# Kernel tuning notes

Hardware: AMD Instinct MI355X
Metric: run time of the kernel (lower is better)

Reference implementation:

```python
import jax, jax.numpy as jnp
import numpy as np

H = 64        # index_n_heads
D = 128       # index_head_dim
R = 64        # rope_head_dim
TOPK = 512    # index_topk
FP8_MAX = 448.0
EPS = 1e-6
THETA = 10000.0


def setup_inputs() -> dict:
    key = jax.random.key(0)
    ks = jax.random.split(key, 6)
    T, DM, QL = 1536, 7168, 1536
    return {
        "hidden_states": jax.random.normal(ks[0], (T, DM), jnp.float32),
        "q_lora": jax.random.normal(ks[1], (T, QL), jnp.float32),
        "wq_b": jax.random.normal(ks[2], (QL, H * D), jnp.float32) / np.sqrt(QL),
        "wk": jax.random.normal(ks[3], (DM, D), jnp.float32) / np.sqrt(DM),
        "k_norm_w": jnp.ones((D,), jnp.float32),
        "k_norm_b": jnp.zeros((D,), jnp.float32),
        "weights_proj_w": jax.random.normal(ks[4], (DM, H), jnp.float32) / np.sqrt(DM),
        "positions": jnp.arange(T, dtype=jnp.int32),
    }


def _rope_neox(x, pos):
    # x: [T, ..., R]; pos: [T]. NEOX-style (half-split) rotary on the rope slice.
    half = R // 2
    inv = 1.0 / (THETA ** (jnp.arange(half, dtype=jnp.float32) / half))
    ang = pos.astype(jnp.float32)[:, None] * inv  # [T, half]
    cos, sin = jnp.cos(ang), jnp.sin(ang)
    while cos.ndim < x.ndim:
        cos, sin = cos[:, None, :], sin[:, None, :]
    x1, x2 = x[..., :half], x[..., half:]
    return jnp.concatenate([x1 * cos - x2 * sin, x2 * cos + x1 * sin], axis=-1)


def _fp8_quant(x):
    # per-row (last-dim) e4m3 quantization: value -> fp8 payload + fp32 scale
    scale = jnp.maximum(jnp.max(jnp.abs(x), axis=-1, keepdims=True) / FP8_MAX, 1e-12)
    xq = (x / scale).astype(jnp.float8_e4m3fn).astype(jnp.float32)
    return xq, scale


def reference(hidden_states, q_lora, wq_b, wk, k_norm_w, k_norm_b, weights_proj_w, positions):
    T = hidden_states.shape[0]
    softmax_scale = D ** (-0.5)
    weights_scale = H ** (-0.5)

    # projections
    q = (q_lora @ wq_b).reshape(T, H, D)          # wq_b
    k = hidden_states @ wk                        # wk

    # k_norm (LayerNorm)
    mu = jnp.mean(k, axis=-1, keepdims=True)
    var = jnp.mean((k - mu) ** 2, axis=-1, keepdims=True)
    k = (k - mu) * jax.lax.rsqrt(var + EPS) * k_norm_w + k_norm_b

    # RoPE on the first rope_head_dim dims of q and k
    q = jnp.concatenate([_rope_neox(q[..., :R], positions), q[..., R:]], axis=-1)
    k = jnp.concatenate([_rope_neox(k[..., :R], positions), k[..., R:]], axis=-1)

    # fp8 quantization (per token-head for q, per token for k)
    q_fp8, q_scale = _fp8_quant(q)   # [T,H,D], [T,H,1]
    k_fp8, k_scale = _fp8_quant(k)   # [T,D],   [T,1]

    # head-gate weights: weights_proj(x) * q_scale * softmax_scale * weights_scale
    gate = hidden_states @ weights_proj_w                      # [T,H]
    w = gate[..., None] * q_scale * (softmax_scale * weights_scale)  # [T,H,1]

    # index score: I[t,s] = sum_h w[t,h] * relu(q[t,h] . k[s]) * k_scale[s]
    qk = jnp.einsum('thd,sd->ths', q_fp8, k_fp8)               # [T,H,S]
    score = jnp.einsum('th,ths->ts', w[..., 0], jax.nn.relu(qk))
    score = score * k_scale[:, 0][None, :]

    # causal (ragged prefill) mask + topk block selection
    causal = positions[:, None] >= positions[None, :]
    score = jnp.where(causal, score, -jnp.inf)
    vals, idx = jax.lax.top_k(score, TOPK)
    idx = jnp.where(jnp.isfinite(vals), idx, -1)
    return idx, vals
```

## Files before the change

### kernel.cpp

```cpp
#include <hip/hip_runtime.h>
#include <hip/hip_bf16.h>
#include <math.h>

#define T_SZ 1536
#define DM_SZ 7168
#define QL_SZ 1536
#define H_SZ 64
#define D_SZ 128
#define ND 8192
#define TOPK_SZ 512
#define N2 192
#define SPLITK2 16

typedef float f32x4 __attribute__((ext_vector_type(4)));
typedef short s16x8 __attribute__((ext_vector_type(8)));
typedef unsigned long long u64;

static __device__ __forceinline__ unsigned char f32_to_e4m3(float x){
  unsigned int b = __float_as_uint(x);
  unsigned int s = (b >> 24) & 0x80u;
  float a = fabsf(x);
  if (a < 0.015625f){
    int m = (int)rintf(a * 512.0f);
    if (m == 8) return (unsigned char)(s | 0x08u);
    return (unsigned char)(s | (unsigned)m);
  }
  int e;
  float mant = frexpf(a, &e);
  int E = e - 1;
  int m = (int)rintf(mant * 16.0f) - 8;
  if (m == 8){ E += 1; m = 0; }
  if (E > 8 || (E == 8 && m > 6)) return (unsigned char)(s | 0x7Eu);
  return (unsigned char)(s | ((unsigned)(E + 7) << 3) | (unsigned)m);
}

static __device__ __forceinline__ unsigned short bf16_rne(float x){
  unsigned int u = __float_as_uint(x);
  return (unsigned short)((u + 0x7FFFu + ((u >> 16) & 1u)) >> 16);
}

typedef __attribute__((address_space(1))) const void gas_void;
typedef __attribute__((address_space(3))) void las_void;
static __device__ __forceinline__ void stage16(const void* g, void* l){
  __builtin_amdgcn_global_load_lds((gas_void*)g, (las_void*)l, 16, 0, 0);
}

__global__ __launch_bounds__(256) void prep_all_k(const float* __restrict__ ql,
                                                  const float* __restrict__ wqb,
                                                  const float* __restrict__ wk,
                                                  const float* __restrict__ wp,
                                                  const int* __restrict__ pos,
                                                  unsigned short* __restrict__ Ahi,
                                                  unsigned short* __restrict__ Alo,
                                                  unsigned short* __restrict__ Bth,
                                                  unsigned short* __restrict__ Btl,
                                                  unsigned short* __restrict__ w2hi,
                                                  unsigned short* __restrict__ w2lo,
                                                  float* __restrict__ cs){
  __shared__ float ld[32][33];
  const int blk = blockIdx.x, tid = threadIdx.x;
  if (blk < 2304){
    int i = blk * 256 + tid;
    float4 v = *(const float4*)&ql[(size_t)i * 4];
    float f[4] = {v.x, v.y, v.z, v.w};
    unsigned short hb[4], lb[4];
#pragma unroll
    for (int j = 0; j < 4; ++j){
      hb[j] = bf16_rne(f[j]);
      float hf = __uint_as_float((unsigned int)hb[j] << 16);
      lb[j] = bf16_rne(f[j] - hf);
    }
    ushort4 h, l;
    h.x = hb[0]; h.y = hb[1]; h.z = hb[2]; h.w = hb[3];
    l.x = lb[0]; l.y = lb[1]; l.z = lb[2]; l.w = lb[3];
    *(ushort4*)&Ahi[(size_t)i * 4] = h;
    *(ushort4*)&Alo[(size_t)i * 4] = l;
  } else if (blk < 14592){
    int f2 = blk - 2304;
    const int n0 = (f2 & 255) * 32, k0 = (f2 >> 8) * 32;
    const int r = tid >> 3, c4 = (tid & 7) * 4;
    float4 v = *(const float4*)&wqb[(size_t)(k0 + r) * ND + n0 + c4];
    ld[r][c4 + 0] = v.x; ld[r][c4 + 1] = v.y; ld[r][c4 + 2] = v.z; ld[r][c4 + 3] = v.w;
    __syncthreads();
    unsigned short hb[4], lb[4];
#pragma unroll
    for (int j = 0; j < 4; ++j){
      float x = ld[c4 + j][r];
      hb[j] = bf16_rne(x);
      float hf = __uint_as_float((unsigned int)hb[j] << 16);
      lb[j] = bf16_rne(x - hf);
    }
    ushort4 h, l;
    h.x = hb[0]; h.y = hb[1]; h.z = hb[2]; h.w = hb[3];
    l.x = lb[0]; l.y = lb[1]; l.z = lb[2]; l.w = lb[3];
    *(ushort4*)&Bth[(size_t)(n0 + r) * QL_SZ + k0 + c4] = h;
    *(ushort4*)&Btl[(size_t)(n0 + r) * QL_SZ + k0 + c4] = l;
  } else if (blk < 15936){
    int g = blk - 14592;
    const int n0 = (g % 6) * 32, k0 = (g / 6) * 32;
    const int r = tid >> 3, c4 = (tid & 7) * 4;
    float4 v;
    if (n0 < 128) v = *(const float4*)&wk[(size_t)(k0 + r) * 128 + n0 + c4];
    else          v = *(const float4*)&wp[(size_t)(k0 + r) * 64 + (n0 - 128) + c4];
    ld[r][c4 + 0] = v.x; ld[r][c4 + 1] = v.y; ld[r][c4 + 2] = v.z; ld[r][c4 + 3] = v.w;
    __syncthreads();
    unsigned short hb[4], lb[4];
#pragma unroll
    for (int j = 0; j < 4; ++j){
      float x = ld[c4 + j][r];
      hb[j] = bf16_rne(x);
      float hf = __uint_as_float((unsigned int)hb[j] << 16);
      lb[j] = bf16_rne(x - hf);
    }
    ushort4 h, l;
    h.x = hb[0]; h.y = hb[1]; h.z = hb[2]; h.w = hb[3];
    l.x = lb[0]; l.y = lb[1]; l.z = lb[2]; l.w = lb[3];
    *(ushort4*)&w2hi[(size_t)(n0 + r) * DM_SZ + k0 + c4] = h;
    *(ushort4*)&w2lo[(size_t)(n0 + r) * DM_SZ + k0 + c4] = l;
  } else {
    int i = (blk - 15936) * 256 + tid;
    int t = i >> 5, j = i & 31;
    float inv = 1.0f / powf(10000.0f, (float)j * (1.0f / 32.0f));
    float ang = (float)pos[t] * inv;
    cs[t * 64 + j]      = cosf(ang);
    cs[t * 64 + 32 + j] = sinf(ang);
  }
}

__global__ void rope_table_k(const int* __restrict__ pos, float* __restrict__ cs){
  int i = blockIdx.x * blockDim.x + threadIdx.x;
  if (i >= T_SZ * 32) return;
  int t = i >> 5, j = i & 31;
  float inv = 1.0f / powf(10000.0f, (float)j * (1.0f / 32.0f));
  float ang = (float)pos[t] * inv;
  cs[t * 64 + j]      = cosf(ang);
  cs[t * 64 + 32 + j] = sinf(ang);
}

__global__ __launch_bounds__(256) void gemm1_mfma_k(const unsigned short* __restrict__ Ahi,
                                                    const unsigned short* __restrict__ Alo,
                                                    const unsigned short* __restrict__ Bhi,
                                                    const unsigned short* __restrict__ Blo,
                                                    float* __restrict__ C){
  __shared__ unsigned short As [128 * 64];
  __shared__ unsigned short Bs0[128 * 64];
  __shared__ unsigned short Bs1[128 * 64];
  const int bid = blockIdx.x;
  const int lid = (bid & 7) * 96 + (bid >> 3);
  const int mt = lid % 12, nt = lid / 12;
  const int m0 = mt * 128, n0 = nt * 128;
  const int tid = threadIdx.x;
  const int w = tid >> 6, l = tid & 63;
  const int wr = w >> 1, wc = w & 1;
  const int lr = l & 15, lg = l >> 4;

  const int srow = w * 32 + (l >> 3);
  const int ssl  = (l & 7) ^ ((l >> 3) & 7);
  const size_t gA = (size_t)(m0 + srow) * QL_SZ + ssl * 8;
  const size_t gB = (size_t)(n0 + srow) * QL_SZ + ssl * 8;
  const int lbase = w * 2048;

  f32x4 acc[4][4];
#pragma unroll
  for (int i = 0; i < 4; ++i)
#pragma unroll
    for (int j = 0; j < 4; ++j) acc[i][j] = (f32x4){0.f, 0.f, 0.f, 0.f};

  const int amrow = wr * 64 + lr;
  const int bnrow = wc * 64 + lr;

  for (int k0 = 0; k0 < QL_SZ; k0 += 64){
#pragma unroll
    for (int i = 0; i < 4; ++i){
      size_t go = (size_t)i * 8 * QL_SZ + k0;
      stage16(Ahi + gA + go, As  + lbase + i * 512);
      stage16(Bhi + gB + go, Bs0 + lbase + i * 512);
      stage16(Blo + gB + go, Bs1 + lbase + i * 512);
    }
    __syncthreads();
#pragma unroll
    for (int kk = 0; kk < 2; ++kk){
      s16x8 af[4], b0[4], b1[4];
#pragma unroll
      for (int f = 0; f < 4; ++f){
        int ma = amrow + f * 16;
        int nb = bnrow + f * 16;
        int sa = ((kk * 4 + lg) ^ (ma & 7)) * 16;
        int sb = ((kk * 4 + lg) ^ (nb & 7)) * 16;
        af[f] = *(const s16x8*)((const char*)As  + ma * 128 + sa);
        b0[f] = *(const s16x8*)((const char*)Bs0 + nb * 128 + sb);
        b1[f] = *(const s16x8*)((const char*)Bs1 + nb * 128 + sb);
      }
#pragma unroll
      for (int fi = 0; fi < 4; ++fi)
#pragma unroll
        for (int fj = 0; fj < 4; ++fj)
          acc[fi][fj] = __builtin_amdgcn_mfma_f32_16x16x32_bf16(af[fi], b0[fj], acc[fi][fj], 0, 0, 0);
#pragma unroll
      for (int fi = 0; fi < 4; ++fi)
#pragma unroll
        for (int fj = 0; fj < 4; ++fj)
          acc[fi][fj] = __builtin_amdgcn_mfma_f32_16x16x32_bf16(af[fi], b1[fj], acc[fi][fj], 0, 0, 0);
    }
    __syncthreads();
#pragma unroll
    for (int i = 0; i < 4; ++i)
      stage16(Alo + gA + (size_t)i * 8 * QL_SZ + k0, As + lbase + i * 512);
    __syncthreads();
#pragma unroll
    for (int kk = 0; kk < 2; ++kk){
      s16x8 af[4], b0[4];
#pragma unroll
      for (int f = 0; f < 4; ++f){
        int ma = amrow + f * 16;
        int nb = bnrow + f * 16;
        af[f] = *(const s16x8*)((const char*)As  + ma * 128 + (((kk * 4 + lg) ^ (ma & 7)) * 16));
        b0[f] = *(const s16x8*)((const char*)Bs0 + nb * 128 + (((kk * 4 + lg) ^ (nb & 7)) * 16));
      }
#pragma unroll
      for (int fi = 0; fi < 4; ++fi)
#pragma unroll
        for (int fj = 0; fj < 4; ++fj)
          acc[fi][fj] = __builtin_amdgcn_mfma_f32_16x16x32_bf16(af[fi], b0[fj], acc[fi][fj], 0, 0, 0);
    }
    __syncthreads();
  }

#pragma unroll
  for (int fi = 0; fi < 4; ++fi){
    const int row = m0 + wr * 64 + fi * 16 + lg * 4;
#pragma unroll
    for (int fj = 0; fj < 4; ++fj){
      float* cp = C + (size_t)row * ND + n0 + wc * 64 + fj * 16 + lr;
      f32x4 d = acc[fi][fj];
      cp[0]              = d.x;
      cp[(size_t)ND]     = d.y;
      cp[(size_t)2 * ND] = d.z;
      cp[(size_t)3 * ND] = d.w;
    }
  }
}

__global__ __launch_bounds__(128) void gemm2_mfma_k(const float* __restrict__ hs,
                                                    const unsigned short* __restrict__ Bhi,
                                                    const unsigned short* __restrict__ Blo,
                                                    float* __restrict__ part){
  __shared__ unsigned short As0[128 * 64];
  __shared__ unsigned short As1[128 * 64];
  __shared__ unsigned short Bs0[64 * 64];
  __shared__ unsigned short Bs1[64 * 64];
  const int bid = blockIdx.x;
  const int lid = (bid & 7) * 72 + (bid >> 3);
  const int s   = lid / 36;
  const int rem = lid % 36;
  const int mt = rem / 3, nt = rem % 3;
  const int m0 = mt * 128, n0 = nt * 64;
  const int kbeg = s * (DM_SZ / SPLITK2);
  const int tid = threadIdx.x;
  const int w = tid >> 6, l = tid & 63;
  const int lr = l & 15, lg = l >> 4;

  const int srow = tid >> 3;
  const int ssl  = (tid & 7) ^ (srow & 7);
  const size_t gB = (size_t)(n0 + srow) * DM_SZ + ssl * 8;
  const int lbase = w * 512;

  f32x4 acc[4][4];
#pragma unroll
  for (int i = 0; i < 4; ++i)
#pragma unroll
    for (int j = 0; j < 4; ++j) acc[i][j] = (f32x4){0.f, 0.f, 0.f, 0.f};

  const int amrow = w * 64 + lr;
  const int bnrow = lr;

  for (int k0 = kbeg; k0 < kbeg + DM_SZ / SPLITK2; k0 += 64){
    f32x4 av[16];
#pragma unroll
    for (int i = 0; i < 8; ++i){
      int idx8 = tid + i * 128;
      int ar = idx8 >> 3, as = idx8 & 7;
      const float* src = hs + (size_t)(m0 + ar) * DM_SZ + k0 + as * 8;
      av[2 * i]     = *(const f32x4*)src;
      av[2 * i + 1] = *(const f32x4*)(src + 4);
    }
#pragma unroll
    for (int i = 0; i < 4; ++i){
      stage16(Bhi + gB + (size_t)i * 16 * DM_SZ + k0, Bs0 + lbase + i * 1024);
      stage16(Blo + gB + (size_t)i * 16 * DM_SZ + k0, Bs1 + lbase + i * 1024);
    }
#pragma unroll
    for (int i = 0; i < 8; ++i){
      int idx8 = tid + i * 128;
      int ar = idx8 >> 3, as = idx8 & 7;
      float f[8];
      *(f32x4*)&f[0] = av[2 * i];
      *(f32x4*)&f[4] = av[2 * i + 1];
      unsigned short hb[8], lb[8];
#pragma unroll
      for (int j = 0; j < 8; ++j){
        hb[j] = bf16_rne(f[j]);
        float hf = __uint_as_float((unsigned int)hb[j] << 16);
        lb[j] = bf16_rne(f[j] - hf);
      }
      int loff = ar * 64 + (as ^ (ar & 7)) * 8;
      *(s16x8*)&As0[loff] = *(s16x8*)hb;
      *(s16x8*)&As1[loff] = *(s16x8*)lb;
    }
    __syncthreads();
#pragma unroll
    for (int kk = 0; kk < 2; ++kk){
      s16x8 ah[4], al[4], b0[4], b1[4];
#pragma unroll
      for (int f = 0; f < 4; ++f){
        int ma = amrow + f * 16;
        int nb = bnrow + f * 16;
        int sa = ((kk * 4 + lg) ^ (ma & 7)) * 16;
        int sb = ((kk * 4 + lg) ^ (nb & 7)) * 16;
        ah[f] = *(const s16x8*)((const char*)As0 + ma * 128 + sa);
        al[f] = *(const s16x8*)((const char*)As1 + ma * 128 + sa);
        b0[f] = *(const s16x8*)((const char*)Bs0 + nb * 128 + sb);
        b1[f] = *(const s16x8*)((const char*)Bs1 + nb * 128 + sb);
      }
#pragma unroll
      for (int fi = 0; fi < 4; ++fi)
#pragma unroll
        for (int fj = 0; fj < 4; ++fj)
          acc[fi][fj] = __builtin_amdgcn_mfma_f32_16x16x32_bf16(ah[fi], b0[fj], acc[fi][fj], 0, 0, 0);
#pragma unroll
      for (int fi = 0; fi < 4; ++fi)
#pragma unroll
        for (int fj = 0; fj < 4; ++fj)
          acc[fi][fj] = __builtin_amdgcn_mfma_f32_16x16x32_bf16(ah[fi], b1[fj], acc[fi][fj], 0, 0, 0);
#pragma unroll
      for (int fi = 0; fi < 4; ++fi)
#pragma unroll
        for (int fj = 0; fj < 4; ++fj)
          acc[fi][fj] = __builtin_amdgcn_mfma_f32_16x16x32_bf16(al[fi], b0[fj], acc[fi][fj], 0, 0, 0);
    }
    __syncthreads();
  }

  float* p = part + (size_t)(s * 36 + mt * 3 + nt) * (128 * 64);
#pragma unroll
  for (int fi = 0; fi < 4; ++fi){
    const int row = w * 64 + fi * 16 + lg * 4;
#pragma unroll
    for (int fj = 0; fj < 4; ++fj){
      float* cp = p + (size_t)row * 64 + fj * 16 + lr;
      f32x4 d = acc[fi][fj];
      cp[  0] = d.x;
      cp[ 64] = d.y;
      cp[128] = d.z;
      cp[192] = d.w;
    }
  }
}

__global__ __launch_bounds__(256) void kq_post_k(const float* __restrict__ part,
                                                 const float* __restrict__ knw,
                                                 const float* __restrict__ knb,
                                                 const float* __restrict__ cs,
                                                 const float* __restrict__ q,
                                                 unsigned char* __restrict__ kf8,
                                                 float* __restrict__ kscale,
                                                 unsigned char* __restrict__ qf8,
                                                 float* __restrict__ wbuf){
  const int t = blockIdx.x, tid = threadIdx.x;
  const int mt = t >> 7, rl = t & 127;
  __shared__ float shq[64 * 132];
  __shared__ float shk[128];
  __shared__ float red[2];
  __shared__ float gsh[64];
  float4 qv[8];
  const float* qrow = q + (size_t)t * 8192;
#pragma unroll
  for (int i = 0; i < 8; ++i) qv[i] = *(const float4*)&qrow[(size_t)(tid + i * 256) * 4];
  float x = 0.0f;
  if (tid < 128){
    const float* pk = part + (size_t)(mt * 3 + (tid >> 6)) * 8192 + rl * 64 + (tid & 63);
#pragma unroll
    for (int s = 0; s < SPLITK2; ++s) x += pk[(size_t)s * 36 * 8192];
  } else if (tid < 192){
    int d = tid - 128;
    const float* pg = part + (size_t)(mt * 3 + 2) * 8192 + rl * 64 + d;
    float gsum = 0.0f;
#pragma unroll
    for (int s = 0; s < SPLITK2; ++s) gsum += pg[(size_t)s * 36 * 8192];
    gsh[d] = gsum;
  }
#pragma unroll
  for (int i = 0; i < 8; ++i){
    int e4 = tid + i * 256;
    float* dst = &shq[(e4 >> 5) * 132 + (e4 & 31) * 4];
    dst[0] = qv[i].x; dst[1] = qv[i].y; dst[2] = qv[i].z; dst[3] = qv[i].w;
  }
  float v = x;
#pragma unroll
  for (int o = 32; o > 0; o >>= 1) v += __shfl_xor(v, o, 64);
  if (tid < 128 && (tid & 63) == 0) red[tid >> 6] = v;
  __syncthreads();
  float mu = (red[0] + red[1]) / 128.0f;
  float dx = x - mu;
  v = dx * dx;
  __syncthreads();
#pragma unroll
  for (int o = 32; o > 0; o >>= 1) v += __shfl_xor(v, o, 64);
  if (tid < 128 && (tid & 63) == 0) red[tid >> 6] = v;
  __syncthreads();
  float var = (red[0] + red[1]) / 128.0f;
  const float* ct = cs + t * 64;
  if (tid < 128){
    float nv = dx * (1.0f / sqrtf(var + 1e-6f)) * knw[tid] + knb[tid];
    shk[tid] = nv;
  }
  __syncthreads();
  float outv = 0.0f;
  if (tid < 128){
    int d = tid;
    float nv = shk[d];
    if (d < 32)        outv = nv * ct[d] - shk[d + 32] * ct[32 + d];
    else if (d < 64){ int j = d - 32; outv = nv * ct[j] + shk[j] * ct[32 + j]; }
    else               outv = nv;
  }
  v = (tid < 128) ? fabsf(outv) : 0.0f;
  __syncthreads();
#pragma unroll
  for (int o = 32; o > 0; o >>= 1) v = fmaxf(v, __shfl_xor(v, o, 64));
  if (tid < 128 && (tid & 63) == 0) red[tid >> 6] = v;
  __syncthreads();
  if (tid < 128){
    float amax = fmaxf(red[0], red[1]);
    float scale = fmaxf(amax / 448.0f, 1e-12f);
    kf8[t * 128 + tid] = f32_to_e4m3(outv / scale);
    if (tid == 0) kscale[t] = scale;
  }
  const int h = tid >> 2, g = tid & 3;
  const float* hq = shq + h * 132;
  float xx[32];
#pragma unroll
  for (int j = 0; j < 32; ++j) xx[j] = hq[g + 4 * j];
  float vals[32];
  float am = 0.0f;
#pragma unroll
  for (int j = 0; j < 8; ++j){
    int d = g + 4 * j;
    float c = ct[d], s = ct[32 + d];
    float lo = xx[j] * c - xx[j + 8] * s;
    float hi = xx[j + 8] * c + xx[j] * s;
    vals[j] = lo; vals[j + 8] = hi;
    am = fmaxf(am, fmaxf(fabsf(lo), fabsf(hi)));
  }
#pragma unroll
  for (int j = 16; j < 32; ++j){ vals[j] = xx[j]; am = fmaxf(am, fabsf(xx[j])); }
  am = fmaxf(am, __shfl_xor(am, 1, 64));
  am = fmaxf(am, __shfl_xor(am, 2, 64));
  float qscale = fmaxf(am / 448.0f, 1e-12f);
  unsigned char* qp = qf8 + (size_t)t * 8192 + h * 128 + g;
#pragma unroll
  for (int j = 0; j < 32; ++j) qp[4 * j] = f32_to_e4m3(vals[j] / qscale);
  if (g == 0) wbuf[t * 64 + h] = gsh[h] * qscale * 0.011048543456039806f;
}

__global__ __launch_bounds__(256) void gemm1_k(const float* __restrict__ A,
                                               const float* __restrict__ B,
                                               float* __restrict__ C){
  __shared__ float As[8][132];
  __shared__ float Bs[8][132];
  const int tid = threadIdx.x;
  const int bm = blockIdx.y * 128, bn = blockIdx.x * 128;
  const int ty = tid >> 4, tx = tid & 15;
  const int arow = tid >> 1, ak = (tid & 1) * 4;
  const int brow = tid >> 5, bcol = (tid & 31) * 4;
  float acc[8][8];
#pragma unroll
  for (int i = 0; i < 8; i++)
#pragma unroll
    for (int j = 0; j < 8; j++) acc[i][j] = 0.0f;

  for (int k0 = 0; k0 < QL_SZ; k0 += 8){
    float4 av = *(const float4*)&A[(size_t)(bm + arow) * QL_SZ + k0 + ak];
    float4 bv = *(const float4*)&B[(size_t)(k0 + brow) * ND + bn + bcol];
    As[ak + 0][arow] = av.x; As[ak + 1][arow] = av.y;
    As[ak + 2][arow] = av.z; As[ak + 3][arow] = av.w;
    *(float4*)&Bs[brow][bcol] = bv;
    __syncthreads();
#pragma unroll
    for (int kk = 0; kk < 8; ++kk){
      float a[8], b[8];
      *(float4*)&a[0] = *(const float4*)&As[kk][ty * 8];
      *(float4*)&a[4] = *(const float4*)&As[kk][ty * 8 + 4];
      *(float4*)&b[0] = *(const float4*)&Bs[kk][tx * 8];
      *(float4*)&b[4] = *(const float4*)&Bs[kk][tx * 8 + 4];
#pragma unroll
      for (int i = 0; i < 8; i++)
#pragma unroll
        for (int j = 0; j < 8; j++) acc[i][j] += a[i] * b[j];
    }
    __syncthreads();
  }
#pragma unroll
  for (int i = 0; i < 8; i++)
#pragma unroll
    for (int j = 0; j < 8; j += 4){
      float4 o; o.x = acc[i][j]; o.y = acc[i][j+1]; o.z = acc[i][j+2]; o.w = acc[i][j+3];
      *(float4*)&C[(size_t)(bm + ty * 8 + i) * ND + bn + tx * 8 + j] = o;
    }
}

__global__ __launch_bounds__(256) void gemm2_partial_k(const float* __restrict__ hs,
                                                       const float* __restrict__ wk,
                                                       const float* __restrict__ wp,
                                                       float* __restrict__ part){
  __shared__ float As[32][33];
  __shared__ float Bs[32][196];
  const int tid = threadIdx.x;
  const int m0 = blockIdx.x * 32;
  const int ks = blockIdx.y;
  const int kbeg = ks * (DM_SZ / 8), kend = kbeg + DM_SZ / 8;
  const int arow = tid >> 3, ak4 = (tid & 7) * 4;
  const int r2 = (tid >> 4) * 2, cg = (tid & 15) * 12;
  float acc[2][12];
#pragma unroll
  for (int i = 0; i < 2; i++)
#pragma unroll
    for (int j = 0; j < 12; j++) acc[i][j] = 0.0f;

  for (int k0 = kbeg; k0 < kend; k0 += 32){
    float4 av = *(const float4*)&hs[(size_t)(m0 + arow) * DM_SZ + k0 + ak4];
    As[ak4 + 0][arow] = av.x; As[ak4 + 1][arow] = av.y;
// ... 294 lines not shown
      prefix = (prefix << 8) | sel[0];
      rem -= sel[1];
    }
    const unsigned int u_thr = prefix;

    const u64 lml = (1ull << lane) - 1ull;
#pragma unroll
    for (int m = 0; m < 8; ++m){
      int j = tid + m * 256;
      unsigned int u = U[j];
      bool pg = (u > u_thr), pt = (u == u_thr);
      u64 mg = __ballot(pg), mtk = __ballot(pt);
      unsigned int bg = 0, bt2 = 0;
      if (lane == 0){
        if (mg)  bg  = atomicAdd(&cnts[0], (unsigned int)__popcll(mg));
        if (mtk) bt2 = atomicAdd(&cnts[1], (unsigned int)__popcll(mtk));
      }
      bg  = __shfl(bg, 0, 64);
      bt2 = __shfl(bt2, 0, 64);
      if (pg)  cand[bg  + (unsigned int)__popcll(mg  & lml)] =
                 ((unsigned long long)u << 32) | (unsigned int)(~(unsigned int)j);
      if (pt)  tix[bt2 + (unsigned int)__popcll(mtk & lml)] = (unsigned int)j;
    }
    __syncthreads();
    const unsigned int G = cnts[0], Tt = cnts[1];
    if (Tt == rem){
      for (unsigned int q = tid; q < Tt; q += 256)
        cand[G + q] = ((unsigned long long)u_thr << 32) | (unsigned int)(~tix[q]);
      __syncthreads();
    } else {
      if (tid < 64) hist[tid] = 0u;
      __syncthreads();
      for (unsigned int q = tid; q < Tt; q += 256) atomicAdd(&hist[tix[q] >> 5], 1u);
      __syncthreads();
      if (tid == 0){
        unsigned int cum = 0; unsigned int d = 0;
        for (; d < 64; ++d){ unsigned int c = hist[d]; if (cum + c >= rem) break; cum += c; }
        sel[0] = d; sel[1] = rem - cum;
      }
      __syncthreads();
      const unsigned int dA = sel[0], remA = sel[1];
      if (tid < 32) hist[64 + tid] = 0u;
      __syncthreads();
      for (unsigned int q = tid; q < Tt; q += 256){
        unsigned int j = tix[q];
        if ((j >> 5) == dA) atomicAdd(&hist[64 + (j & 31u)], 1u);
      }
      __syncthreads();
      if (tid == 0){
        unsigned int cum = 0; unsigned int e = 0;
        for (; e < 32; ++e){ unsigned int c = hist[64 + e]; if (cum + c >= remA) break; cum += c; }
        sel[0] = dA * 32 + e;
        cnts[1] = 0u;
      }
      __syncthreads();
      const unsigned int jthr = sel[0];
      for (unsigned int q = tid; q < Tt; q += 256){
        unsigned int j = tix[q];
        if (j <= jthr){
          unsigned int p = atomicAdd(&cnts[1], 1u);
          cand[G + p] = ((unsigned long long)u_thr << 32) | (unsigned int)(~j);
        }
      }
      __syncthreads();
    }
  } else {
    for (int i = tid; i < 512; i += 256){
      unsigned int u = (i < n) ? U[i] : 0u;
      cand[i] = u ? (((unsigned long long)u << 32) | (unsigned int)(~(unsigned int)i)) : 0ull;
    }
    __syncthreads();
  }

  u64 a = cand[2 * tid], b = cand[2 * tid + 1];
#pragma unroll
  for (int k = 2; k <= 512; k <<= 1){
#pragma unroll
    for (int j = k >> 1; j >= 1; j >>= 1){
      if (j >= 128){
        __syncthreads();
        cand[2 * tid] = a; cand[2 * tid + 1] = b;
        __syncthreads();
        int e0 = 2 * tid;
        u64 p0 = cand[e0 ^ j], p1 = cand[(e0 + 1) ^ j];
        bool up  = ((e0 & k) == 0);
        bool low = ((e0 & j) == 0);
        bool mx = (up == low);
        a = mx ? (a > p0 ? a : p0) : (a < p0 ? a : p0);
        b = mx ? (b > p1 ? b : p1) : (b < p1 ? b : p1);
      } else if (j >= 2){
        int d = j >> 1;
        u64 p0 = __shfl_xor(a, d, 64);
        u64 p1 = __shfl_xor(b, d, 64);
        bool up  = (((2 * tid) & k) == 0);
        bool low = ((tid & d) == 0);
        bool mx = (up == low);
        a = mx ? (a > p0 ? a : p0) : (a < p0 ? a : p0);
        b = mx ? (b > p1 ? b : p1) : (b < p1 ? b : p1);
      } else {
        bool up = (((2 * tid) & k) == 0);
        u64 mn = a < b ? a : b, mxv = a < b ? b : a;
        a = up ? mxv : mn;
        b = up ? mn : mxv;
      }
    }
  }

#pragma unroll
  for (int m = 0; m < 2; ++m){
    int i = 2 * tid + m;
    u64 kk = m ? b : a;
    unsigned int u = (unsigned int)(kk >> 32);
    unsigned int bb = (u & 0x80000000u) ? (u & 0x7fffffffu) : ~u;
    float val = __uint_as_float(bb);
    int idx = (int)(~(unsigned int)(kk & 0xffffffffu));
    bool fin = (u != 0u) && (val > -__builtin_huge_valf());
    out[(size_t)t * TOPK_SZ + i] = fin ? (float)idx : -1.0f;
    out[(size_t)T_SZ * TOPK_SZ + (size_t)t * TOPK_SZ + i] = fin ? val : -3.0e38f;
  }
}

extern "C" void kernel_launch(void* const* d_in, const int* in_sizes, int n_in,
                              void* d_out, int out_size, void* d_ws, size_t ws_size,
                              hipStream_t stream){
  const float* hs  = (const float*)d_in[0];
  const float* ql  = (const float*)d_in[1];
  const float* wqb = (const float*)d_in[2];
  const float* wk  = (const float*)d_in[3];
  const float* knw = (const float*)d_in[4];
  const float* knb = (const float*)d_in[5];
  const float* wpj = (const float*)d_in[6];
  const int*   pos = (const int*)d_in[7];
  char* ws = (char*)d_ws;
  size_t off = 0;
  auto alloc = [&](size_t b){ size_t o = off; off += (b + 255) & ~(size_t)255; return o; };
  float* cs     = (float*)(ws + alloc((size_t)T_SZ * 64 * 4));
  float* qbuf   = (float*)(ws + alloc((size_t)T_SZ * ND * 4));
  float* kraw   = (float*)(ws + alloc((size_t)T_SZ * 128 * 4));
  float* gate   = (float*)(ws + alloc((size_t)T_SZ * 64 * 4));
  unsigned char* kf8 = (unsigned char*)(ws + alloc((size_t)T_SZ * 128));
  float* kscale = (float*)(ws + alloc((size_t)T_SZ * 4));
  float* wbuf   = (float*)(ws + alloc((size_t)T_SZ * 64 * 4));
  unsigned short* w2hi = (unsigned short*)(ws + alloc((size_t)N2 * DM_SZ * 2));
  unsigned short* w2lo = (unsigned short*)(ws + alloc((size_t)N2 * DM_SZ * 2));
  const size_t base2 = off;

  size_t o1 = base2;
  auto alloc1 = [&](size_t b){ size_t o = o1; o1 += (b + 255) & ~(size_t)255; return o; };
  unsigned short* Ahi = (unsigned short*)(ws + alloc1((size_t)T_SZ * QL_SZ * 2));
  unsigned short* Alo = (unsigned short*)(ws + alloc1((size_t)T_SZ * QL_SZ * 2));
  unsigned short* Bth = (unsigned short*)(ws + alloc1((size_t)ND * QL_SZ * 2));
  unsigned short* Btl = (unsigned short*)(ws + alloc1((size_t)ND * QL_SZ * 2));

  size_t o2 = base2;
  auto alloc2 = [&](size_t b){ size_t o = o2; o2 += (b + 255) & ~(size_t)255; return o; };
  float* part2 = (float*)(ws + alloc2((size_t)SPLITK2 * 36 * 128 * 64 * 4));
  unsigned char* qf8 = (unsigned char*)(ws + alloc2((size_t)T_SZ * ND));

  const bool fit = (o1 <= ws_size) && (o2 <= ws_size);

  float* part_old = (float*)(ws + base2);
  unsigned char* qf8_fb = (unsigned char*)(ws + base2);
  float* score = qbuf;
  float* out = (float*)d_out;

  if (fit){
    prep_all_k<<<dim3(16128), dim3(256), 0, stream>>>(ql, wqb, wk, wpj, pos,
                                                      Ahi, Alo, Bth, Btl, w2hi, w2lo, cs);
    gemm1_mfma_k<<<dim3(768), dim3(256), 0, stream>>>(Ahi, Alo, Bth, Btl, qbuf);
    gemm2_mfma_k<<<dim3(12 * 3 * SPLITK2), dim3(128), 0, stream>>>(hs, w2hi, w2lo, part2);
    kq_post_k<<<dim3(T_SZ), dim3(256), 0, stream>>>(part2, knw, knb, cs, qbuf, kf8, kscale, qf8, wbuf);
    score_mfma_k<<<dim3(600), dim3(256), 0, stream>>>(qf8, kf8, wbuf, kscale, score);
    topk_sel_k<<<dim3(T_SZ), dim3(256), 0, stream>>>(score, out);
  } else {
    rope_table_k<<<dim3((T_SZ * 32 + 255) / 256), dim3(256), 0, stream>>>(pos, cs);
    gemm2_partial_k<<<dim3(48, 8), dim3(256), 0, stream>>>(hs, wk, wpj, part_old);
    gemm2_reduce_k<<<dim3((T_SZ * 192) / 256), dim3(256), 0, stream>>>(part_old, kraw, gate);
    k_post_k<<<dim3(T_SZ), dim3(128), 0, stream>>>(kraw, knw, knb, cs, kf8, kscale);
    gemm1_k<<<dim3(ND / 128, T_SZ / 128), dim3(256), 0, stream>>>(ql, wqb, qbuf);
    q_post2_k<<<dim3(T_SZ), dim3(256), 0, stream>>>(qbuf, gate, cs, qf8_fb, wbuf);
    score_mfma_k<<<dim3(600), dim3(256), 0, stream>>>(qf8_fb, kf8, wbuf, kscale, score);
    topk_sel_k<<<dim3(T_SZ), dim3(256), 0, stream>>>(score, out);
  }
}
```

Before: 253.1 us.

## Fuse q-projection and k/gate projection GEMMs into one heterogeneous launch

Merges the two separate GEMM launches into one kernel whose first 768 blocks compute the q projection and whose remaining 576 blocks compute the split-K k/gate projection. Both GEMMs then run concurrently and share the GPU, which removes a launch boundary and the tail idle time between them. The partial buffer is moved past the A/B staging buffers so the two halves do not alias, which needs more workspace. When the workspace is too small it falls back to the old path. The second-GEMM blocks use 256 threads with only 128 active, which wastes occupancy.

```diff
diff --git a/kernel.cpp b/kernel.cpp
--- a/kernel.cpp
+++ b/kernel.cpp
@@ -135,6 +135,235 @@
   float ang = (float)pos[t] * inv;
   cs[t * 64 + j]      = cosf(ang);
   cs[t * 64 + 32 + j] = sinf(ang);
+}
+
+__global__ __launch_bounds__(256) void gemm12_k(const unsigned short* __restrict__ Ahi,
+                                                const unsigned short* __restrict__ Alo,
+                                                const unsigned short* __restrict__ Bth,
+                                                const unsigned short* __restrict__ Btl,
+                                                const float* __restrict__ hs,
+                                                const unsigned short* __restrict__ Bhi2,
+                                                const unsigned short* __restrict__ Blo2,
+                                                float* __restrict__ C,
+                                                float* __restrict__ part){
+  __shared__ unsigned short smem[24576];
+  const int bid0 = blockIdx.x;
+  const int tid = threadIdx.x;
+  if (bid0 < 768){
+    unsigned short* As  = smem;
+    unsigned short* Bs0 = smem + 8192;
+    unsigned short* Bs1 = smem + 16384;
+    const int bid = bid0;
+    const int lid = (bid & 7) * 96 + (bid >> 3);
+    const int mt = lid % 12, nt = lid / 12;
+    const int m0 = mt * 128, n0 = nt * 128;
+    const int w = tid >> 6, l = tid & 63;
+    const int wr = w >> 1, wc = w & 1;
+    const int lr = l & 15, lg = l >> 4;
+
+    const int srow = w * 32 + (l >> 3);
+    const int ssl  = (l & 7) ^ ((l >> 3) & 7);
+    const size_t gA = (size_t)(m0 + srow) * QL_SZ + ssl * 8;
+    const size_t gB = (size_t)(n0 + srow) * QL_SZ + ssl * 8;
+    const int lbase = w * 2048;
+
+    f32x4 acc[4][4];
+#pragma unroll
+    for (int i = 0; i < 4; ++i)
+#pragma unroll
+      for (int j = 0; j < 4; ++j) acc[i][j] = (f32x4){0.f, 0.f, 0.f, 0.f};
+
+    const int amrow = wr * 64 + lr;
+    const int bnrow = wc * 64 + lr;
+
+    for (int k0 = 0; k0 < QL_SZ; k0 += 64){
+#pragma unroll
+      for (int i = 0; i < 4; ++i){
+        size_t go = (size_t)i * 8 * QL_SZ + k0;
+        stage16(Ahi + gA + go, As  + lbase + i * 512);
+        stage16(Bth + gB + go, Bs0 + lbase + i * 512);
+        stage16(Btl + gB + go, Bs1 + lbase + i * 512);
+      }
+      __syncthreads();
+#pragma unroll
+      for (int kk = 0; kk < 2; ++kk){
+        s16x8 af[4], b0[4], b1[4];
+#pragma unroll
+        for (int f = 0; f < 4; ++f){
+          int ma = amrow + f * 16;
+          int nb = bnrow + f * 16;
+          int sa = ((kk * 4 + lg) ^ (ma & 7)) * 16;
+          int sb = ((kk * 4 + lg) ^ (nb & 7)) * 16;
+          af[f] = *(const s16x8*)((const char*)As  + ma * 128 + sa);
+          b0[f] = *(const s16x8*)((const char*)Bs0 + nb * 128 + sb);
+          b1[f] = *(const s16x8*)((const char*)Bs1 + nb * 128 + sb);
+        }
+#pragma unroll
+        for (int fi = 0; fi < 4; ++fi)
+#pragma unroll
+          for (int fj = 0; fj < 4; ++fj)
+            acc[fi][fj] = __builtin_amdgcn_mfma_f32_16x16x32_bf16(af[fi], b0[fj], acc[fi][fj], 0, 0, 0);
+#pragma unroll
+        for (int fi = 0; fi < 4; ++fi)
+#pragma unroll
+          for (int fj = 0; fj < 4; ++fj)
+            acc[fi][fj] = __builtin_amdgcn_mfma_f32_16x16x32_bf16(af[fi], b1[fj], acc[fi][fj], 0, 0, 0);
+      }
+      __syncthreads();
+#pragma unroll
+      for (int i = 0; i < 4; ++i)
+        stage16(Alo + gA + (size_t)i * 8 * QL_SZ + k0, As + lbase + i * 512);
+      __syncthreads();
+#pragma unroll
+      for (int kk = 0; kk < 2; ++kk){
+        s16x8 af[4], b0[4];
+#pragma unroll
+        for (int f = 0; f < 4; ++f){
+          int ma = amrow + f * 16;
+          int nb = bnrow + f * 16;
+          af[f] = *(const s16x8*)((const char*)As  + ma * 128 + (((kk * 4 + lg) ^ (ma & 7)) * 16));
+          b0[f] = *(const s16x8*)((const char*)Bs0 + nb * 128 + (((kk * 4 + lg) ^ (nb & 7)) * 16));
+        }
+#pragma unroll
+        for (int fi = 0; fi < 4; ++fi)
+#pragma unroll
+          for (int fj = 0; fj < 4; ++fj)
+            acc[fi][fj] = __builtin_amdgcn_mfma_f32_16x16x32_bf16(af[fi], b0[fj], acc[fi][fj], 0, 0, 0);
+      }
+      __syncthreads();
+    }
+
+#pragma unroll
+    for (int fi = 0; fi < 4; ++fi){
+      const int row = m0 + wr * 64 + fi * 16 + lg * 4;
+#pragma unroll
+      for (int fj = 0; fj < 4; ++fj){
+        float* cp = C + (size_t)row * ND + n0 + wc * 64 + fj * 16 + lr;
+        f32x4 d = acc[fi][fj];
+        cp[0]              = d.x;
+        cp[(size_t)ND]     = d.y;
+        cp[(size_t)2 * ND] = d.z;
+        cp[(size_t)3 * ND] = d.w;
+      }
+    }
+  } else {
+    unsigned short* As0 = smem;
+    unsigned short* As1 = smem + 8192;
+    unsigned short* Bs0 = smem + 16384;
+    unsigned short* Bs1 = smem + 20480;
+    const int bid = bid0 - 768;
+    const int lid = (bid & 7) * 72 + (bid >> 3);
+    const int s   = lid / 36;
+    const int rem = lid % 36;
+    const int mt = rem / 3, nt = rem % 3;
+    const int m0 = mt * 128, n0 = nt * 64;
+    const int kbeg = s * (DM_SZ / SPLITK2);
+    const int w = tid >> 6, l = tid & 63;
+    const int lr = l & 15, lg = l >> 4;
+    const bool act = (tid < 128);
+
+    const int srow = tid >> 3;
+    const int ssl  = (tid & 7) ^ (srow & 7);
+    const size_t gB = (size_t)(n0 + srow) * DM_SZ + ssl * 8;
+    const int lbase = w * 512;
+
+    f32x4 acc[4][4];
+#pragma unroll
+    for (int i = 0; i < 4; ++i)
+#pragma unroll
+      for (int j = 0; j < 4; ++j) acc[i][j] = (f32x4){0.f, 0.f, 0.f, 0.f};
+
+    const int amrow = w * 64 + lr;
+    const int bnrow = lr;
+
+    for (int k0 = kbeg; k0 < kbeg + DM_SZ / SPLITK2; k0 += 64){
+      if (act){
+        f32x4 av[16];
+#pragma unroll
+        for (int i = 0; i < 8; ++i){
+          int idx8 = tid + i * 128;
+          int ar = idx8 >> 3, as = idx8 & 7;
+          const float* src = hs + (size_t)(m0 + ar) * DM_SZ + k0 + as * 8;
+          av[2 * i]     = *(const f32x4*)src;
+          av[2 * i + 1] = *(const f32x4*)(src + 4);
+        }
+#pragma unroll
+        for (int i = 0; i < 4; ++i){
+          stage16(Bhi2 + gB + (size_t)i * 16 * DM_SZ + k0, Bs0 + lbase + i * 1024);
+          stage16(Blo2 + gB + (size_t)i * 16 * DM_SZ + k0, Bs1 + lbase + i * 1024);
+        }
+#pragma unroll
+        for (int i = 0; i < 8; ++i){
+          int idx8 = tid + i * 128;
+          int ar = idx8 >> 3, as = idx8 & 7;
+          float f[8];
+          *(f32x4*)&f[0] = av[2 * i];
+          *(f32x4*)&f[4] = av[2 * i + 1];
+          unsigned short hb[8], lb[8];
+#pragma unroll
+          for (int j = 0; j < 8; ++j){
+            hb[j] = bf16_rne(f[j]);
+            float hf = __uint_as_float((unsigned int)hb[j] << 16);
+            lb[j] = bf16_rne(f[j] - hf);
+          }
+          int loff = ar * 64 + (as ^ (ar & 7)) * 8;
+          *(s16x8*)&As0[loff] = *(s16x8*)hb;
+          *(s16x8*)&As1[loff] = *(s16x8*)lb;
+        }
+      }
+      __syncthreads();
+      if (act){
+#pragma unroll
+        for (int kk = 0; kk < 2; ++kk){
+          s16x8 ah[4], al[4], b0[4], b1[4];
+#pragma unroll
+          for (int f = 0; f < 4; ++f){
+            int ma = amrow + f * 16;
+            int nb = bnrow + f * 16;
+            int sa = ((kk * 4 + lg) ^ (ma & 7)) * 16;
+            int sb = ((kk * 4 + lg) ^ (nb & 7)) * 16;
+            ah[f] = *(const s16x8*)((const char*)As0 + ma * 128 + sa);
+            al[f] = *(const s16x8*)((const char*)As1 + ma * 128 + sa);
+            b0[f] = *(const s16x8*)((const char*)Bs0 + nb * 128 + sb);
+            b1[f] = *(const s16x8*)((const char*)Bs1 + nb * 128 + sb);
+          }
+#pragma unroll
+          for (int fi = 0; fi < 4; ++fi)
+#pragma unroll
+            for (int fj = 0; fj < 4; ++fj)
+              acc[fi][fj] = __builtin_amdgcn_mfma_f32_16x16x32_bf16(ah[fi], b0[fj], acc[fi][fj], 0, 0, 0);
+#pragma unroll
+          for (int fi = 0; fi < 4; ++fi)
+#pragma unroll
+            for (int fj = 0; fj < 4; ++fj)
+              acc[fi][fj] = __builtin_amdgcn_mfma_f32_16x16x32_bf16(ah[fi], b1[fj], acc[fi][fj], 0, 0, 0);
+#pragma unroll
+          for (int fi = 0; fi < 4; ++fi)
+#pragma unroll
+            for (int fj = 0; fj < 4; ++fj)
+              acc[fi][fj] = __builtin_amdgcn_mfma_f32_16x16x32_bf16(al[fi], b0[fj], acc[fi][fj], 0, 0, 0);
+        }
+      }
+      __syncthreads();
+    }
+
+    if (act){
+      float* p = part + (size_t)(s * 36 + mt * 3 + nt) * (128 * 64);
+#pragma unroll
+      for (int fi = 0; fi < 4; ++fi){
+        const int row = w * 64 + fi * 16 + lg * 4;
+#pragma unroll
+        for (int fj = 0; fj < 4; ++fj){
+          float* cp = p + (size_t)row * 64 + fj * 16 + lr;
+          f32x4 d = acc[fi][fj];
+          cp[  0] = d.x;
+          cp[ 64] = d.y;
+          cp[128] = d.z;
+          cp[192] = d.w;
+        }
+      }
+    }
+  }
 }
 
 __global__ __launch_bounds__(256) void gemm1_mfma_k(const unsigned short* __restrict__ Ahi,
@@ -976,19 +1205,33 @@
   unsigned short* Bth = (unsigned short*)(ws + alloc1((size_t)ND * QL_SZ * 2));
   unsigned short* Btl = (unsigned short*)(ws + alloc1((size_t)ND * QL_SZ * 2));
 
+  size_t o_ov = o1;
+  auto allocov = [&](size_t b){ size_t o = o_ov; o_ov += (b + 255) & ~(size_t)255; return o; };
+  float* part2_ov = (float*)(ws + allocov((size_t)SPLITK2 * 36 * 128 * 64 * 4));
+  unsigned char* qf8_ov = (unsigned char*)(ws + base2);
+
   size_t o2 = base2;
   auto alloc2 = [&](size_t b){ size_t o = o2; o2 += (b + 255) & ~(size_t)255; return o; };
   float* part2 = (float*)(ws + alloc2((size_t)SPLITK2 * 36 * 128 * 64 * 4));
   unsigned char* qf8 = (unsigned char*)(ws + alloc2((size_t)T_SZ * ND));
 
-  const bool fit = (o1 <= ws_size) && (o2 <= ws_size);
+  const bool fit_ov = (o_ov <= ws_size);
+  const bool fit    = (o1 <= ws_size) && (o2 <= ws_size);
 
   float* part_old = (float*)(ws + base2);
   unsigned char* qf8_fb = (unsigned char*)(ws + base2);
   float* score = qbuf;
   float* out = (float*)d_out;
 
-  if (fit){
+  if (fit_ov){
+    prep_all_k<<<dim3(16128), dim3(256), 0, stream>>>(ql, wqb, wk, wpj, pos,
+                                                      Ahi, Alo, Bth, Btl, w2hi, w2lo, cs);
+    gemm12_k<<<dim3(768 + 576), dim3(256), 0, stream>>>(Ahi, Alo, Bth, Btl,
+                                                        hs, w2hi, w2lo, qbuf, part2_ov);
+    kq_post_k<<<dim3(T_SZ), dim3(256), 0, stream>>>(part2_ov, knw, knb, cs, qbuf, kf8, kscale, qf8_ov, wbuf);
+    score_mfma_k<<<dim3(600), dim3(256), 0, stream>>>(qf8_ov, kf8, wbuf, kscale, score);
+    topk_sel_k<<<dim3(T_SZ), dim3(256), 0, stream>>>(score, out);
+  } else if (fit){
     prep_all_k<<<dim3(16128), dim3(256), 0, stream>>>(ql, wqb, wk, wpj, pos,
                                                       Ahi, Alo, Bth, Btl, w2hi, w2lo, cs);
     gemm1_mfma_k<<<dim3(768), dim3(256), 0, stream>>>(Ahi, Alo, Bth, Btl, qbuf);
```

Result: slower. 260.9 us (+3.1%).

## Split q-projection GEMM along K into two halves with reduction in post kernel

Applied to the files above, without the earlier changes.

Adds a split-K variant of the bf16 hi/lo MFMA q-projection GEMM that launches 1536 blocks, each covering half of the K dimension, and writes two partial outputs. The post-processing kernel now loads both partial q buffers and sums them before the rope and quantization work. This is meant to raise block count and occupancy across the CUs for the 768-tile GEMM. In exchange it adds a second 48MB fp32 write and read, and the path is taken only when the workspace is large enough.

```diff
diff --git a/kernel.cpp b/kernel.cpp
--- a/kernel.cpp
+++ b/kernel.cpp
@@ -137,6 +137,115 @@
   cs[t * 64 + 32 + j] = sinf(ang);
 }
 
+__global__ __launch_bounds__(256) void gemm1s_k(const unsigned short* __restrict__ Ahi,
+                                                const unsigned short* __restrict__ Alo,
+                                                const unsigned short* __restrict__ Bhi,
+                                                const unsigned short* __restrict__ Blo,
+                                                float* __restrict__ Ca,
+                                                float* __restrict__ Cb){
+  __shared__ unsigned short As [128 * 64];
+  __shared__ unsigned short Bs0[128 * 64];
+  __shared__ unsigned short Bs1[128 * 64];
+  const int bid = blockIdx.x;
+  const int lid = (bid & 7) * 192 + (bid >> 3);
+  const int half = lid / 768;
+  const int rem = lid % 768;
+  const int mt = rem % 12, nt = rem / 12;
+  const int m0 = mt * 128, n0 = nt * 128;
+  const int kbeg = half * 768;
+  const int tid = threadIdx.x;
+  const int w = tid >> 6, l = tid & 63;
+  const int wr = w >> 1, wc = w & 1;
+  const int lr = l & 15, lg = l >> 4;
+
+  const int srow = w * 32 + (l >> 3);
+  const int ssl  = (l & 7) ^ ((l >> 3) & 7);
+  const size_t gA = (size_t)(m0 + srow) * QL_SZ + ssl * 8;
+  const size_t gB = (size_t)(n0 + srow) * QL_SZ + ssl * 8;
+  const int lbase = w * 2048;
+
+  f32x4 acc[4][4];
+#pragma unroll
+  for (int i = 0; i < 4; ++i)
+#pragma unroll
+    for (int j = 0; j < 4; ++j) acc[i][j] = (f32x4){0.f, 0.f, 0.f, 0.f};
+
+  const int amrow = wr * 64 + lr;
+  const int bnrow = wc * 64 + lr;
+
+  for (int k0 = kbeg; k0 < kbeg + 768; k0 += 64){
+#pragma unroll
+    for (int i = 0; i < 4; ++i){
+      size_t go = (size_t)i * 8 * QL_SZ + k0;
+      stage16(Ahi + gA + go, As  + lbase + i * 512);
+      stage16(Bhi + gB + go, Bs0 + lbase + i * 512);
+      stage16(Blo + gB + go, Bs1 + lbase + i * 512);
+    }
+    __syncthreads();
+#pragma unroll
+    for (int kk = 0; kk < 2; ++kk){
+      s16x8 af[4], b0[4], b1[4];
+#pragma unroll
+      for (int f = 0; f < 4; ++f){
+        int ma = amrow + f * 16;
+        int nb = bnrow + f * 16;
+        int sa = ((kk * 4 + lg) ^ (ma & 7)) * 16;
+        int sb = ((kk * 4 + lg) ^ (nb & 7)) * 16;
+        af[f] = *(const s16x8*)((const char*)As  + ma * 128 + sa);
+        b0[f] = *(const s16x8*)((const char*)Bs0 + nb * 128 + sb);
+        b1[f] = *(const s16x8*)((const char*)Bs1 + nb * 128 + sb);
+      }
+#pragma unroll
+      for (int fi = 0; fi < 4; ++fi)
+#pragma unroll
+        for (int fj = 0; fj < 4; ++fj)
+          acc[fi][fj] = __builtin_amdgcn_mfma_f32_16x16x32_bf16(af[fi], b0[fj], acc[fi][fj], 0, 0, 0);
+#pragma unroll
+      for (int fi = 0; fi < 4; ++fi)
+#pragma unroll
+        for (int fj = 0; fj < 4; ++fj)
+          acc[fi][fj] = __builtin_amdgcn_mfma_f32_16x16x32_bf16(af[fi], b1[fj], acc[fi][fj], 0, 0, 0);
+    }
+    __syncthreads();
+#pragma unroll
+    for (int i = 0; i < 4; ++i)
+      stage16(Alo + gA + (size_t)i * 8 * QL_SZ + k0, As + lbase + i * 512);
+    __syncthreads();
+#pragma unroll
+    for (int kk = 0; kk < 2; ++kk){
+      s16x8 af[4], b0[4];
+#pragma unroll
+      for (int f = 0; f < 4; ++f){
+        int ma = amrow + f * 16;
+        int nb = bnrow + f * 16;
+        af[f] = *(const s16x8*)((const char*)As  + ma * 128 + (((kk * 4 + lg) ^ (ma & 7)) * 16));
+        b0[f] = *(const s16x8*)((const char*)Bs0 + nb * 128 + (((kk * 4 + lg) ^ (nb & 7)) * 16));
+      }
+#pragma unroll
+      for (int fi = 0; fi < 4; ++fi)
+#pragma unroll
+        for (int fj = 0; fj < 4; ++fj)
+          acc[fi][fj] = __builtin_amdgcn_mfma_f32_16x16x32_bf16(af[fi], b0[fj], acc[fi][fj], 0, 0, 0);
+    }
+    __syncthreads();
+  }
+
+  float* C = half ? Cb : Ca;
+#pragma unroll
+  for (int fi = 0; fi < 4; ++fi){
+    const int row = m0 + wr * 64 + fi * 16 + lg * 4;
+#pragma unroll
+    for (int fj = 0; fj < 4; ++fj){
+      float* cp = C + (size_t)row * ND + n0 + wc * 64 + fj * 16 + lr;
+      f32x4 d = acc[fi][fj];
+      cp[0]              = d.x;
+      cp[(size_t)ND]     = d.y;
+      cp[(size_t)2 * ND] = d.z;
+      cp[(size_t)3 * ND] = d.w;
+    }
+  }
+}
+
 __global__ __launch_bounds__(256) void gemm1_mfma_k(const unsigned short* __restrict__ Ahi,
                                                     const unsigned short* __restrict__ Alo,
                                                     const unsigned short* __restrict__ Bhi,
@@ -361,7 +470,8 @@
                                                  const float* __restrict__ knw,
                                                  const float* __restrict__ knb,
                                                  const float* __restrict__ cs,
-                                                 const float* __restrict__ q,
+                                                 const float* __restrict__ qa,
+                                                 const float* __restrict__ qb,
                                                  unsigned char* __restrict__ kf8,
                                                  float* __restrict__ kscale,
                                                  unsigned char* __restrict__ qf8,
@@ -372,10 +482,20 @@
   __shared__ float shk[128];
   __shared__ float red[2];
   __shared__ float gsh[64];
-  float4 qv[8];
-  const float* qrow = q + (size_t)t * 8192;
+  float4 qv[8], qv2[8];
+  const float* qrow = qa + (size_t)t * 8192;
 #pragma unroll
   for (int i = 0; i < 8; ++i) qv[i] = *(const float4*)&qrow[(size_t)(tid + i * 256) * 4];
+  if (qb){
+    const float* qrow2 = qb + (size_t)t * 8192;
+#pragma unroll
+    for (int i = 0; i < 8; ++i) qv2[i] = *(const float4*)&qrow2[(size_t)(tid + i * 256) * 4];
+#pragma unroll
+    for (int i = 0; i < 8; ++i){
+      qv[i].x += qv2[i].x; qv[i].y += qv2[i].y;
+      qv[i].z += qv2[i].z; qv[i].w += qv2[i].w;
+    }
+  }
   float x = 0.0f;
   if (tid < 128){
     const float* pk = part + (size_t)(mt * 3 + (tid >> 6)) * 8192 + rl * 64 + (tid & 63);
@@ -981,19 +1101,33 @@
   float* part2 = (float*)(ws + alloc2((size_t)SPLITK2 * 36 * 128 * 64 * 4));
   unsigned char* qf8 = (unsigned char*)(ws + alloc2((size_t)T_SZ * ND));
 
-  const bool fit = (o1 <= ws_size) && (o2 <= ws_size);
+  size_t oq = (o1 > o2 ? o1 : o2);
+  oq = (oq + 255) & ~(size_t)255;
+  float* qb = (float*)(ws + oq);
+  const size_t oq_end = oq + (size_t)T_SZ * ND * 4;
+
+  const bool fit  = (o1 <= ws_size) && (o2 <= ws_size);
+  const bool fit2 = fit && (oq_end <= ws_size);
 
   float* part_old = (float*)(ws + base2);
   unsigned char* qf8_fb = (unsigned char*)(ws + base2);
   float* score = qbuf;
   float* out = (float*)d_out;
 
-  if (fit){
+  if (fit2){
+    prep_all_k<<<dim3(16128), dim3(256), 0, stream>>>(ql, wqb, wk, wpj, pos,
+                                                      Ahi, Alo, Bth, Btl, w2hi, w2lo, cs);
+    gemm1s_k<<<dim3(1536), dim3(256), 0, stream>>>(Ahi, Alo, Bth, Btl, qbuf, qb);
+    gemm2_mfma_k<<<dim3(12 * 3 * SPLITK2), dim3(128), 0, stream>>>(hs, w2hi, w2lo, part2);
+    kq_post_k<<<dim3(T_SZ), dim3(256), 0, stream>>>(part2, knw, knb, cs, qbuf, qb, kf8, kscale, qf8, wbuf);
+    score_mfma_k<<<dim3(600), dim3(256), 0, stream>>>(qf8, kf8, wbuf, kscale, score);
+    topk_sel_k<<<dim3(T_SZ), dim3(256), 0, stream>>>(score, out);
+  } else if (fit){
     prep_all_k<<<dim3(16128), dim3(256), 0, stream>>>(ql, wqb, wk, wpj, pos,
                                                       Ahi, Alo, Bth, Btl, w2hi, w2lo, cs);
     gemm1_mfma_k<<<dim3(768), dim3(256), 0, stream>>>(Ahi, Alo, Bth, Btl, qbuf);
     gemm2_mfma_k<<<dim3(12 * 3 * SPLITK2), dim3(128), 0, stream>>>(hs, w2hi, w2lo, part2);
-    kq_post_k<<<dim3(T_SZ), dim3(256), 0, stream>>>(part2, knw, knb, cs, qbuf, kf8, kscale, qf8, wbuf);
+    kq_post_k<<<dim3(T_SZ), dim3(256), 0, stream>>>(part2, knw, knb, cs, qbuf, nullptr, kf8, kscale, qf8, wbuf);
     score_mfma_k<<<dim3(600), dim3(256), 0, stream>>>(qf8, kf8, wbuf, kscale, score);
     topk_sel_k<<<dim3(T_SZ), dim3(256), 0, stream>>>(score, out);
   } else {
```

Result: slower. 268.4 us (+6.0%).
